# Kernel tuning notes

Measured on AMD Instinct MI355X. Metric: run time of the kernel, lower is better.

The kernel has to match this reference:

```python
import jax, jax.numpy as jnp
import numpy as np

# --- config (matches init_kwargs) ---
C = 1e-12
FILTER_LENGTH = 512
INPUT_SIZE = 8192
NUM_LAYERS = 4
BATCH = 4096

MIN_NORM = 1e-15
PROJ_EPS = 4e-3  # hgcn PoincareBall eps for float32


def _proj(x, c):
    # clip points to stay inside the Poincare ball
    norm = jnp.maximum(jnp.linalg.norm(x, axis=-1, keepdims=True), MIN_NORM)
    maxnorm = (1.0 - PROJ_EPS) / jnp.sqrt(c)
    return jnp.where(norm > maxnorm, x / norm * maxnorm, x)


def _expmap0(u, c):
    # proj_tan0 is identity on the Poincare ball
    sqrt_c = jnp.sqrt(c)
    u_norm = jnp.maximum(jnp.linalg.norm(u, axis=-1, keepdims=True), MIN_NORM)
    return jnp.tanh(sqrt_c * u_norm) * u / (sqrt_c * u_norm)


def _mobius_add(x, y, c):
    x2 = jnp.sum(x * x, axis=-1, keepdims=True)
    y2 = jnp.sum(y * y, axis=-1, keepdims=True)
    xy = jnp.sum(x * y, axis=-1, keepdims=True)
    num = (1.0 + 2.0 * c * xy + c * y2) * x + (1.0 - c * x2) * y
    denom = 1.0 + 2.0 * c * xy + c * c * x2 * y2
    return num / jnp.maximum(denom, MIN_NORM)


def setup_inputs() -> dict:
    key = jax.random.key(0)
    ks = jax.random.split(key, 2 + NUM_LAYERS)
    inp = {
        "hk": jax.random.normal(ks[0], (BATCH, INPUT_SIZE), dtype=jnp.float32),
        # torch.rand -> uniform [0,1)
        "w": jax.random.uniform(ks[1], (NUM_LAYERS, FILTER_LENGTH), dtype=jnp.float32),
    }
    for i in range(NUM_LAYERS):
        inp[f"bk{i}"] = jax.random.uniform(
            ks[2 + i], (INPUT_SIZE + (i + 1) * FILTER_LENGTH,), dtype=jnp.float32
        )
    return inp


def reference(hk, w, bk0, bk1, bk2, bk3):
    bks = [bk0, bk1, bk2, bk3]
    # full 1D convolution, batched over rows: out[b, j] = sum_l w[j-l] * v[b, l]
    conv1 = jax.vmap(lambda v, wi: jnp.convolve(v, wi, mode="full"), in_axes=(0, None))
    out = hk
    for i in range(NUM_LAYERS):
        v = out[:, :INPUT_SIZE]          # expansive_conv reads only first INPUT_SIZE entries
        conv = conv1(v, w[i])            # [B, INPUT_SIZE + FILTER_LENGTH - 1]
        pad = i * FILTER_LENGTH + 1      # zero tail up to conv_length = INPUT_SIZE + (i+1)*FL
        conv = jnp.pad(conv, ((0, 0), (0, pad)))
        hyp = _proj(_expmap0(conv, C), C)
        out = jax.nn.relu(_mobius_add(hyp, bks[i][None, :], C))
    return out
```

## Files before the change

kernel.cpp:

```cpp
#include <hip/hip_runtime.h>
#include <hip/hip_bf16.h>
#include <math.h>

#define TB 448
#define NW 7
#define TPW 5
#define VOFFH 512
#define SVH 9760
#define UMAX 49

typedef __attribute__((ext_vector_type(8))) short bf16x8;
typedef __attribute__((ext_vector_type(4))) float f32x4;

__device__ __forceinline__ short f2b(float x) {
    union { __hip_bfloat16 h; short s; } u;
    u.h = __float2bfloat16(x);
    return u.s;
}

__global__ __launch_bounds__(256) void y2_kernel(
    const float* __restrict__ bk0, const float* __restrict__ bk1,
    const float* __restrict__ bk2, const float* __restrict__ bk3,
    float* __restrict__ ws)
{
    const float* bks[4] = {bk0, bk1, bk2, bk3};
    const int i = blockIdx.x;
    const int L = 8192 + (i + 1) * 512;
    const float* b = bks[i];
    float s = 0.f;
    for (int n = threadIdx.x; n < L; n += 256) { float x = b[n]; s += x * x; }
    #pragma unroll
    for (int off = 32; off; off >>= 1) s += __shfl_down(s, off, 64);
    __shared__ float sp[4];
    if ((threadIdx.x & 63) == 0) sp[threadIdx.x >> 6] = s;
    __syncthreads();
    if (threadIdx.x == 0) ws[i] = sp[0] + sp[1] + sp[2] + sp[3];
}

__global__ __launch_bounds__(64) void prep_kernel(const float* __restrict__ w,
                                                  short* __restrict__ wtab)
{
    const int id   = blockIdx.x;
    const int layer = id / 17, ks = id % 17;
    const int lane = threadIdx.x;
    const int r    = lane & 15;
    const int kb   = ks * 32 + (lane >> 4) * 8;
    const float* wl = w + layer * 512;
    bf16x8 bb;
    #pragma unroll
    for (int jj = 0; jj < 8; ++jj) {
        const int idx = 512 + r - (kb + jj);
        const float val = (idx >= 0 && idx < 512) ? wl[idx] : 0.f;
        bb[jj] = f2b(val);
    }
    *(bf16x8*)(wtab + ((size_t)id * 64 + lane) * 8) = bb;
}

__global__ __launch_bounds__(TB, 4) void hdcnn_kernel(
    const float* __restrict__ hk, const short* __restrict__ wtab,
    const float* __restrict__ bk0, const float* __restrict__ bk1,
    const float* __restrict__ bk2, const float* __restrict__ bk3,
    const float* __restrict__ y2w, float* __restrict__ out)
{
    __shared__ __align__(16) short svb[SVH];
    __shared__ float sred[NW * 2];

    const int tid  = threadIdx.x;
    const int row  = blockIdx.x;
    const int lane = tid & 63;
    const int wv   = tid >> 6;
    const int jn   = lane & 15;
    const int kq   = lane >> 4;
    const int t0   = wv * TPW;

    {
        int* svi = (int*)svb;
        for (int i = tid; i < SVH / 2; i += TB) svi[i] = 0;
    }
    __syncthreads();

    {
        const float4* hrow = (const float4*)(hk + (size_t)row * 8192);
        for (int j = tid; j < 1024; j += TB) {
            float4 x0 = hrow[2 * j];
            float4 x1 = hrow[2 * j + 1];
            bf16x8 p;
            p[0] = f2b(x0.x); p[1] = f2b(x0.y); p[2] = f2b(x0.z); p[3] = f2b(x0.w);
            p[4] = f2b(x1.x); p[5] = f2b(x1.y); p[6] = f2b(x1.z); p[7] = f2b(x1.w);
            *(bf16x8*)(svb + VOFFH + 8 * j) = p;
        }
    }

    const int vbase = t0 * 256 + 16 * jn + 8 * kq;

    for (int layer = 0; layer < 4; ++layer) {
        const float* __restrict__ bk = (layer == 0) ? bk0 : (layer == 1) ? bk1
                                     : (layer == 2) ? bk2 : bk3;

        const short* wt = wtab + (size_t)layer * 8704 + lane * 8;
        bf16x8 wf[17];
        #pragma unroll
        for (int ks = 0; ks < 17; ++ks) wf[ks] = *(const bf16x8*)(wt + ks * 512);

        __syncthreads();

        f32x4 acc[TPW];
        #pragma unroll
        for (int dt = 0; dt < TPW; ++dt) acc[dt] = (f32x4){0.f, 0.f, 0.f, 0.f};

        #pragma unroll
        for (int u = 0; u < UMAX; ++u) {
            bf16x8 vf = *(const bf16x8*)(svb + vbase + 32 * u);
            const int dtlo = (u > 16) ? ((u - 9) >> 3) : 0;
            const int dthi = ((u >> 3) < TPW - 1) ? (u >> 3) : (TPW - 1);
            #pragma unroll
            for (int dt = dtlo; dt <= dthi; ++dt)
                acc[dt] = __builtin_amdgcn_mfma_f32_16x16x32_bf16(
                    wf[u - 8 * dt], vf, acc[dt], 0, 0, 0);
        }

        float sum2 = 0.f, sxy = 0.f;
        #pragma unroll
        for (int dt = 0; dt < TPW; ++dt) {
            if (t0 + dt < 34) {
                const int nb = (t0 + dt) * 256 + 16 * jn + 4 * kq;
                float4 b4 = *(const float4*)(bk + nb);
                sum2 = fmaf(acc[dt][0], acc[dt][0], sum2);
                sum2 = fmaf(acc[dt][1], acc[dt][1], sum2);
                sum2 = fmaf(acc[dt][2], acc[dt][2], sum2);
                sum2 = fmaf(acc[dt][3], acc[dt][3], sum2);
                sxy  = fmaf(acc[dt][0], b4.x, sxy);
                sxy  = fmaf(acc[dt][1], b4.y, sxy);
                sxy  = fmaf(acc[dt][2], b4.z, sxy);
                sxy  = fmaf(acc[dt][3], b4.w, sxy);
            }
        }
        #pragma unroll
        for (int off = 32; off; off >>= 1) {
            sum2 += __shfl_down(sum2, off, 64);
            sxy  += __shfl_down(sxy,  off, 64);
        }
        if (lane == 0) { sred[wv * 2] = sum2; sred[wv * 2 + 1] = sxy; }
        __syncthreads();
        float un2 = 0.f, xys = 0.f;
        #pragma unroll
        for (int i = 0; i < NW; ++i) { un2 += sred[2 * i]; xys += sred[2 * i + 1]; }

        const float Cc  = 1e-12f;
        const float un  = sqrtf(un2);
        const float unc = fmaxf(un, 1e-15f);
        const float aa  = 1e-6f * unc;
        const float f   = tanhf(aa) / aa;
        const float hn  = f * un;
        const float hnc = fmaxf(hn, 1e-15f);
        const float maxn = (1.0f - 0.004f) * 1.0e6f;
        const float s   = (hnc > maxn) ? f * (maxn / hnc) : f;
        const float x2  = s * s * un2;
        const float xy  = s * xys;
        const float y2  = y2w[layer];
        const float t2c = 2.f * Cc * xy;
        const float A   = 1.f + t2c + Cc * y2;
        const float B   = 1.f - Cc * x2;
        float D = 1.f + t2c + Cc * Cc * x2 * y2;
        D = fmaxf(D, 1e-15f);
        const float alpha = A * s / D;
        const float beta  = B / D;

        if (layer < 3) {
            #pragma unroll
            for (int dt = 0; dt < TPW; ++dt) {
                if (t0 + dt < 32) {
                    const int nb = (t0 + dt) * 256 + 16 * jn + 4 * kq;
                    float4 b4 = *(const float4*)(bk + nb);
                    short4 o;
                    o.x = f2b(fmaxf(alpha * acc[dt][0] + beta * b4.x, 0.f));
                    o.y = f2b(fmaxf(alpha * acc[dt][1] + beta * b4.y, 0.f));
                    o.z = f2b(fmaxf(alpha * acc[dt][2] + beta * b4.z, 0.f));
                    o.w = f2b(fmaxf(alpha * acc[dt][3] + beta * b4.w, 0.f));
                    *(short4*)(svb + VOFFH + nb) = o;
                }
            }
        } else {
            float* orow = out + (size_t)row * 10240;
            #pragma unroll
            for (int dt = 0; dt < TPW; ++dt) {
                if (t0 + dt < 34) {
                    const int nb = (t0 + dt) * 256 + 16 * jn + 4 * kq;
                    float4 b4 = *(const float4*)(bk + nb);
                    float4 o;
                    o.x = fmaxf(alpha * acc[dt][0] + beta * b4.x, 0.f);
                    o.y = fmaxf(alpha * acc[dt][1] + beta * b4.y, 0.f);
                    o.z = fmaxf(alpha * acc[dt][2] + beta * b4.z, 0.f);
                    o.w = fmaxf(alpha * acc[dt][3] + beta * b4.w, 0.f);
                    *(float4*)(orow + nb) = o;
                }
            }
            for (int n = 8704 + 4 * tid; n < 10240; n += 4 * TB) {
                float4 b4 = *(const float4*)(bk + n);
                float4 o;
                o.x = fmaxf(beta * b4.x, 0.f);
                o.y = fmaxf(beta * b4.y, 0.f);
                o.z = fmaxf(beta * b4.z, 0.f);
                o.w = fmaxf(beta * b4.w, 0.f);
                *(float4*)(orow + n) = o;
            }
        }
    }
}

extern "C" void kernel_launch(void* const* d_in, const int* in_sizes, int n_in,
                              void* d_out, int out_size, void* d_ws, size_t ws_size,
                              hipStream_t stream) {
    const float* hk  = (const float*)d_in[0];
    const float* w   = (const float*)d_in[1];
    const float* bk0 = (const float*)d_in[2];
    const float* bk1 = (const float*)d_in[3];
    const float* bk2 = (const float*)d_in[4];
    const float* bk3 = (const float*)d_in[5];
    float* out = (float*)d_out;
    float* ws  = (float*)d_ws;
    short* wtab = (short*)(ws + 4);

    y2_kernel<<<4, 256, 0, stream>>>(bk0, bk1, bk2, bk3, ws);
    prep_kernel<<<68, 64, 0, stream>>>(w, wtab);
    hdcnn_kernel<<<4096, TB, 0, stream>>>(hk, wtab, bk0, bk1, bk2, bk3, ws, out);
}
```

Before: 256.3 us.

## Prefetch next-layer weights and bias early, fold reductions into MFMA loop

Moves the per-layer weight-fragment loads so the next layer's filter fragments are fetched right after the current MFMA loop, overlapping them with the reduction and barrier. Bias vectors are loaded inside the MFMA loop as soon as each tile begins and kept in registers for the epilogue, so the second bias read is gone. Each tile's contribution to the sum-of-squares and dot-product reductions is folded in as soon as the tile finishes accumulating. This aims to hide global-load latency and cut duplicate loads, at the cost of more live registers, which may pressure the launch-bounds occupancy target.

```diff
diff --git a/kernel.cpp b/kernel.cpp
--- a/kernel.cpp
+++ b/kernel.cpp
@@ -16,6 +16,18 @@
     union { __hip_bfloat16 h; short s; } u;
     u.h = __float2bfloat16(x);
     return u.s;
+}
+
+__device__ __forceinline__ void fold4(const f32x4& a, const float4& b,
+                                      float& s2, float& sx) {
+    s2 = fmaf(a[0], a[0], s2);
+    s2 = fmaf(a[1], a[1], s2);
+    s2 = fmaf(a[2], a[2], s2);
+    s2 = fmaf(a[3], a[3], s2);
+    sx = fmaf(a[0], b.x, sx);
+    sx = fmaf(a[1], b.y, sx);
+    sx = fmaf(a[2], b.z, sx);
+    sx = fmaf(a[3], b.w, sx);
 }
 
 __global__ __launch_bounds__(256) void y2_kernel(
@@ -92,21 +104,26 @@
     }
 
     const int vbase = t0 * 256 + 16 * jn + 8 * kq;
+    const int nbb   = t0 * 256 + 16 * jn + 4 * kq;
+
+    bf16x8 wf[17];
+    {
+        const short* wt = wtab + lane * 8;
+        #pragma unroll
+        for (int ks = 0; ks < 17; ++ks) wf[ks] = *(const bf16x8*)(wt + ks * 512);
+    }
 
     for (int layer = 0; layer < 4; ++layer) {
         const float* __restrict__ bk = (layer == 0) ? bk0 : (layer == 1) ? bk1
                                      : (layer == 2) ? bk2 : bk3;
 
-        const short* wt = wtab + (size_t)layer * 8704 + lane * 8;
-        bf16x8 wf[17];
-        #pragma unroll
-        for (int ks = 0; ks < 17; ++ks) wf[ks] = *(const bf16x8*)(wt + ks * 512);
-
         __syncthreads();
 
         f32x4 acc[TPW];
         #pragma unroll
         for (int dt = 0; dt < TPW; ++dt) acc[dt] = (f32x4){0.f, 0.f, 0.f, 0.f};
+        float4 b40, b41, b42, b43, b44;
+        float sum2 = 0.f, sxy = 0.f;
 
         #pragma unroll
         for (int u = 0; u < UMAX; ++u) {
@@ -117,24 +134,24 @@
             for (int dt = dtlo; dt <= dthi; ++dt)
                 acc[dt] = __builtin_amdgcn_mfma_f32_16x16x32_bf16(
                     wf[u - 8 * dt], vf, acc[dt], 0, 0, 0);
-        }
-
-        float sum2 = 0.f, sxy = 0.f;
-        #pragma unroll
-        for (int dt = 0; dt < TPW; ++dt) {
-            if (t0 + dt < 34) {
-                const int nb = (t0 + dt) * 256 + 16 * jn + 4 * kq;
-                float4 b4 = *(const float4*)(bk + nb);
-                sum2 = fmaf(acc[dt][0], acc[dt][0], sum2);
-                sum2 = fmaf(acc[dt][1], acc[dt][1], sum2);
-                sum2 = fmaf(acc[dt][2], acc[dt][2], sum2);
-                sum2 = fmaf(acc[dt][3], acc[dt][3], sum2);
-                sxy  = fmaf(acc[dt][0], b4.x, sxy);
-                sxy  = fmaf(acc[dt][1], b4.y, sxy);
-                sxy  = fmaf(acc[dt][2], b4.z, sxy);
-                sxy  = fmaf(acc[dt][3], b4.w, sxy);
-            }
-        }
+            if (u == 1  && t0 + 0 < 34) b40 = *(const float4*)(bk + nbb);
+            if (u == 9  && t0 + 1 < 34) b41 = *(const float4*)(bk + nbb + 256);
+            if (u == 17 && t0 + 2 < 34) b42 = *(const float4*)(bk + nbb + 512);
+            if (u == 25 && t0 + 3 < 34) b43 = *(const float4*)(bk + nbb + 768);
+            if (u == 33 && t0 + 4 < 34) b44 = *(const float4*)(bk + nbb + 1024);
+            if (u == 16 && t0 + 0 < 34) fold4(acc[0], b40, sum2, sxy);
+            if (u == 24 && t0 + 1 < 34) fold4(acc[1], b41, sum2, sxy);
+            if (u == 32 && t0 + 2 < 34) fold4(acc[2], b42, sum2, sxy);
+            if (u == 40 && t0 + 3 < 34) fold4(acc[3], b43, sum2, sxy);
+            if (u == 48 && t0 + 4 < 34) fold4(acc[4], b44, sum2, sxy);
+        }
+
+        if (layer < 3) {
+            const short* wt = wtab + (size_t)(layer + 1) * 8704 + lane * 8;
+            #pragma unroll
+            for (int ks = 0; ks < 17; ++ks) wf[ks] = *(const bf16x8*)(wt + ks * 512);
+        }
+
         #pragma unroll
         for (int off = 32; off; off >>= 1) {
             sum2 += __shfl_down(sum2, off, 64);
@@ -167,33 +184,87 @@
         const float beta  = B / D;
 
         if (layer < 3) {
-            #pragma unroll
-            for (int dt = 0; dt < TPW; ++dt) {
-                if (t0 + dt < 32) {
-                    const int nb = (t0 + dt) * 256 + 16 * jn + 4 * kq;
-                    float4 b4 = *(const float4*)(bk + nb);
-                    short4 o;
-                    o.x = f2b(fmaxf(alpha * acc[dt][0] + beta * b4.x, 0.f));
-                    o.y = f2b(fmaxf(alpha * acc[dt][1] + beta * b4.y, 0.f));
-                    o.z = f2b(fmaxf(alpha * acc[dt][2] + beta * b4.z, 0.f));
-                    o.w = f2b(fmaxf(alpha * acc[dt][3] + beta * b4.w, 0.f));
-                    *(short4*)(svb + VOFFH + nb) = o;
-                }
+            if (t0 + 0 < 32) {
+                short4 o;
+                o.x = f2b(fmaxf(alpha * acc[0][0] + beta * b40.x, 0.f));
+                o.y = f2b(fmaxf(alpha * acc[0][1] + beta * b40.y, 0.f));
+                o.z = f2b(fmaxf(alpha * acc[0][2] + beta * b40.z, 0.f));
+                o.w = f2b(fmaxf(alpha * acc[0][3] + beta * b40.w, 0.f));
+                *(short4*)(svb + VOFFH + nbb) = o;
+            }
+            if (t0 + 1 < 32) {
+                short4 o;
+                o.x = f2b(fmaxf(alpha * acc[1][0] + beta * b41.x, 0.f));
+                o.y = f2b(fmaxf(alpha * acc[1][1] + beta * b41.y, 0.f));
+                o.z = f2b(fmaxf(alpha * acc[1][2] + beta * b41.z, 0.f));
+                o.w = f2b(fmaxf(alpha * acc[1][3] + beta * b41.w, 0.f));
+                *(short4*)(svb + VOFFH + nbb + 256) = o;
+            }
+            if (t0 + 2 < 32) {
+                short4 o;
+                o.x = f2b(fmaxf(alpha * acc[2][0] + beta * b42.x, 0.f));
+                o.y = f2b(fmaxf(alpha * acc[2][1] + beta * b42.y, 0.f));
+                o.z = f2b(fmaxf(alpha * acc[2][2] + beta * b42.z, 0.f));
+                o.w = f2b(fmaxf(alpha * acc[2][3] + beta * b42.w, 0.f));
+                *(short4*)(svb + VOFFH + nbb + 512) = o;
+            }
+            if (t0 + 3 < 32) {
+                short4 o;
+                o.x = f2b(fmaxf(alpha * acc[3][0] + beta * b43.x, 0.f));
+                o.y = f2b(fmaxf(alpha * acc[3][1] + beta * b43.y, 0.f));
+                o.z = f2b(fmaxf(alpha * acc[3][2] + beta * b43.z, 0.f));
+                o.w = f2b(fmaxf(alpha * acc[3][3] + beta * b43.w, 0.f));
+                *(short4*)(svb + VOFFH + nbb + 768) = o;
+            }
+            if (t0 + 4 < 32) {
+                short4 o;
+                o.x = f2b(fmaxf(alpha * acc[4][0] + beta * b44.x, 0.f));
+                o.y = f2b(fmaxf(alpha * acc[4][1] + beta * b44.y, 0.f));
+                o.z = f2b(fmaxf(alpha * acc[4][2] + beta * b44.z, 0.f));
+                o.w = f2b(fmaxf(alpha * acc[4][3] + beta * b44.w, 0.f));
+                *(short4*)(svb + VOFFH + nbb + 1024) = o;
             }
         } else {
             float* orow = out + (size_t)row * 10240;
-            #pragma unroll
-            for (int dt = 0; dt < TPW; ++dt) {
-                if (t0 + dt < 34) {
-                    const int nb = (t0 + dt) * 256 + 16 * jn + 4 * kq;
-                    float4 b4 = *(const float4*)(bk + nb);
-                    float4 o;
-                    o.x = fmaxf(alpha * acc[dt][0] + beta * b4.x, 0.f);
-                    o.y = fmaxf(alpha * acc[dt][1] + beta * b4.y, 0.f);
-                    o.z = fmaxf(alpha * acc[dt][2] + beta * b4.z, 0.f);
-                    o.w = fmaxf(alpha * acc[dt][3] + beta * b4.w, 0.f);
-                    *(float4*)(orow + nb) = o;
-                }
+            if (t0 + 0 < 34) {
+                float4 o;
+                o.x = fmaxf(alpha * acc[0][0] + beta * b40.x, 0.f);
+                o.y = fmaxf(alpha * acc[0][1] + beta * b40.y, 0.f);
+                o.z = fmaxf(alpha * acc[0][2] + beta * b40.z, 0.f);
+                o.w = fmaxf(alpha * acc[0][3] + beta * b40.w, 0.f);
+                *(float4*)(orow + nbb) = o;
+            }
+            if (t0 + 1 < 34) {
+                float4 o;
+                o.x = fmaxf(alpha * acc[1][0] + beta * b41.x, 0.f);
+                o.y = fmaxf(alpha * acc[1][1] + beta * b41.y, 0.f);
+                o.z = fmaxf(alpha * acc[1][2] + beta * b41.z, 0.f);
+                o.w = fmaxf(alpha * acc[1][3] + beta * b41.w, 0.f);
+                *(float4*)(orow + nbb + 256) = o;
+            }
+            if (t0 + 2 < 34) {
+                float4 o;
+                o.x = fmaxf(alpha * acc[2][0] + beta * b42.x, 0.f);
+                o.y = fmaxf(alpha * acc[2][1] + beta * b42.y, 0.f);
+                o.z = fmaxf(alpha * acc[2][2] + beta * b42.z, 0.f);
+                o.w = fmaxf(alpha * acc[2][3] + beta * b42.w, 0.f);
+                *(float4*)(orow + nbb + 512) = o;
+            }
+            if (t0 + 3 < 34) {
+                float4 o;
+                o.x = fmaxf(alpha * acc[3][0] + beta * b43.x, 0.f);
+                o.y = fmaxf(alpha * acc[3][1] + beta * b43.y, 0.f);
+                o.z = fmaxf(alpha * acc[3][2] + beta * b43.z, 0.f);
+                o.w = fmaxf(alpha * acc[3][3] + beta * b43.w, 0.f);
+                *(float4*)(orow + nbb + 768) = o;
+            }
+            if (t0 + 4 < 34) {
+                float4 o;
+                o.x = fmaxf(alpha * acc[4][0] + beta * b44.x, 0.f);
+                o.y = fmaxf(alpha * acc[4][1] + beta * b44.y, 0.f);
+                o.z = fmaxf(alpha * acc[4][2] + beta * b44.z, 0.f);
+                o.w = fmaxf(alpha * acc[4][3] + beta * b44.w, 0.f);
+                *(float4*)(orow + nbb + 1024) = o;
             }
             for (int n = 8704 + 4 * tid; n < 10240; n += 4 * TB) {
                 float4 b4 = *(const float4*)(bk + n);
```

Result: slower. 276.0 us (+7.7%).
